# Performance work log

Measured on AMD Instinct MI355X. Metric: run time of the kernel, lower is better.

Reference implementation:

```python
import jax, jax.numpy as jnp
import numpy as np


def setup_inputs() -> dict:
    key = jax.random.key(0)
    k_fm, k_idx, k_x, k_y = jax.random.split(key, 4)
    N, C, H, W = 4, 256, 200, 272
    R = 1000
    feature_map = jax.random.normal(k_fm, (N, C, H, W), dtype=jnp.float32)
    img_idx = jax.random.randint(k_idx, (R,), 0, N, dtype=jnp.int32)
    # inclusive coords: x1<=x2<W, y1<=y2<H
    xs = jnp.sort(jax.random.randint(k_x, (R, 2), 0, W, dtype=jnp.int32), axis=1)
    ys = jnp.sort(jax.random.randint(k_y, (R, 2), 0, H, dtype=jnp.int32), axis=1)
    rois = jnp.stack([img_idx, xs[:, 0], ys[:, 0], xs[:, 1], ys[:, 1]], axis=1)
    return {"feature_map": feature_map, "rois": rois, "output_size": 7}


def reference(feature_map, rois, output_size):
    """ROI pooling with torch AdaptiveAvgPool2d semantics per crop.

    Bin i of a length-L crop averages rows [floor(i*L/O), ceil((i+1)*L/O)).
    Implemented exactly and fully vectorized via a 2D integral image, so no
    Python loop over ROIs and no dynamic shapes.
    """
    N, C, H, W = feature_map.shape
    O = output_size
    # integral image, zero-padded: integ[n,c,h,w] = sum of feature_map[n,c,:h,:w]
    integ = jnp.pad(
        jnp.cumsum(jnp.cumsum(feature_map, axis=2), axis=3),
        ((0, 0), (0, 0), (1, 0), (1, 0)),
    )
    img_idx = rois[:, 0]
    x1, y1, x2, y2 = rois[:, 1], rois[:, 2], rois[:, 3], rois[:, 4]
    h_in = y2 - y1 + 1  # inclusive coords -> crop size [R]
    w_in = x2 - x1 + 1
    b = jnp.arange(O, dtype=rois.dtype)
    # adaptive-pool bin edges (start inclusive, end exclusive), shape [R,O]
    hs = y1[:, None] + (b * h_in[:, None]) // O
    he = y1[:, None] + ((b + 1) * h_in[:, None] + O - 1) // O  # ceil div
    ws = x1[:, None] + (b * w_in[:, None]) // O
    we = x1[:, None] + ((b + 1) * w_in[:, None] + O - 1) // O
    n = img_idx[:, None, None]  # [R,1,1]

    def corner(hi, wi):
        # -> [R, O, O, C]
        return integ[n, :, hi[:, :, None], wi[:, None, :]]

    sums = corner(he, we) - corner(hs, we) - corner(he, ws) + corner(hs, ws)
    area = ((he - hs)[:, :, None] * (we - ws)[:, None, :]).astype(feature_map.dtype)
    out = (sums / area[..., None]).transpose(0, 3, 1, 2)  # [R, C, O, O]
    return img_idx, out
```

## Files before the change

### kernel.cpp

```cpp
#include <hip/hip_runtime.h>

#define NIMG 4
#define CCH  256
#define HDIM 200
#define WDIM 272
#define OSZ  7

__global__ __launch_bounds__(256) void k_rowscan(const float* __restrict__ fm,
                                                 float* __restrict__ integ) {
    const int c = threadIdx.x;
    const int b = blockIdx.x;
    const int n = b / HDIM;
    const int h = b % HDIM;

    const float4* src = reinterpret_cast<const float4*>(
        fm + ((size_t)((n * CCH + c) * HDIM + h)) * WDIM);
    float* dst = integ + ((size_t)(n * HDIM + h) * WDIM) * CCH + c;

    float acc = 0.0f;
#pragma unroll 4
    for (int w4 = 0; w4 < WDIM / 4; ++w4) {
        float4 v = src[w4];
        float a0 = acc + v.x;
        float a1 = a0 + v.y;
        float a2 = a1 + v.z;
        float a3 = a2 + v.w;
        size_t wb = (size_t)(w4 * 4) * CCH;
        dst[wb]            = a0;
        dst[wb + CCH]      = a1;
        dst[wb + 2 * CCH]  = a2;
        dst[wb + 3 * CCH]  = a3;
        acc = a3;
    }
}

__global__ __launch_bounds__(256) void k_colscan(float4* __restrict__ integ4) {
    const int C4 = CCH / 4;
    int t = blockIdx.x * 256 + threadIdx.x;
    int c4 = t & (C4 - 1);
    int rest = t >> 6;
    int w = rest % WDIM;
    int n = rest / WDIM;

    const int stride = WDIM * C4;
    int idx = ((n * HDIM) * WDIM + w) * C4 + c4;

    float4 run = make_float4(0.f, 0.f, 0.f, 0.f);
    for (int h = 0; h < HDIM; h += 2) {
        float4 v0 = integ4[idx];
        float4 v1 = integ4[idx + stride];
        run.x += v0.x; run.y += v0.y; run.z += v0.z; run.w += v0.w;
        integ4[idx] = run;
        run.x += v1.x; run.y += v1.y; run.z += v1.z; run.w += v1.w;
        integ4[idx + stride] = run;
        idx += 2 * stride;
    }
}

__global__ __launch_bounds__(256) void k_pool(const float* __restrict__ integ,
                                              const int* __restrict__ rois,
                                              float* __restrict__ out, int R) {
    const int b  = blockIdx.x;
    const int r  = b / (OSZ * OSZ);
    const int ij = b % (OSZ * OSZ);
    const int i  = ij / OSZ;
    const int j  = ij % OSZ;
    const int c  = threadIdx.x;

    const int* rp = rois + r * 5;
    const int n  = rp[0];
    const int x1 = rp[1], y1 = rp[2], x2 = rp[3], y2 = rp[4];
    const int h_in = y2 - y1 + 1;
    const int w_in = x2 - x1 + 1;

    const int hs = y1 + (i * h_in) / OSZ;
    const int he = y1 + ((i + 1) * h_in + OSZ - 1) / OSZ;
    const int ws = x1 + (j * w_in) / OSZ;
    const int we = x1 + ((j + 1) * w_in + OSZ - 1) / OSZ;

    const float inv_area = 1.0f / (float)((he - hs) * (we - ws));

    const int hi = he - 1, hl = hs - 1;
    const int wi = we - 1, wl = ws - 1;

    const float* base = integ + (size_t)n * HDIM * WDIM * CCH + c;

    float A = base[((size_t)hi * WDIM + wi) * CCH];
    float B = (hl >= 0) ? base[((size_t)hl * WDIM + wi) * CCH] : 0.0f;
    float Cv = (wl >= 0) ? base[((size_t)hi * WDIM + wl) * CCH] : 0.0f;
    float D = (hl >= 0 && wl >= 0) ? base[((size_t)hl * WDIM + wl) * CCH] : 0.0f;

    float s = (A - B) - (Cv - D);
    out[R + (((size_t)r * CCH + c) * OSZ + i) * OSZ + j] = s * inv_area;

    if (ij == 0 && c == 0) out[r] = (float)n;
}

__global__ __launch_bounds__(256) void k_direct(const float* __restrict__ fm,
                                                const int* __restrict__ rois,
                                                float* __restrict__ out, int R) {
    const int b  = blockIdx.x;
    const int r  = b / (OSZ * OSZ);
    const int ij = b % (OSZ * OSZ);
    const int i  = ij / OSZ;
    const int j  = ij % OSZ;
    const int c  = threadIdx.x;

    const int* rp = rois + r * 5;
    const int n  = rp[0];
    const int x1 = rp[1], y1 = rp[2], x2 = rp[3], y2 = rp[4];
    const int h_in = y2 - y1 + 1;
    const int w_in = x2 - x1 + 1;

    const int hs = y1 + (i * h_in) / OSZ;
    const int he = y1 + ((i + 1) * h_in + OSZ - 1) / OSZ;
    const int ws = x1 + (j * w_in) / OSZ;
    const int we = x1 + ((j + 1) * w_in + OSZ - 1) / OSZ;

    const float inv_area = 1.0f / (float)((he - hs) * (we - ws));

    const float* p = fm + (size_t)(n * CCH + c) * HDIM * WDIM;
    float acc = 0.0f;
    for (int h = hs; h < he; ++h) {
        const float* row = p + (size_t)h * WDIM;
        for (int w = ws; w < we; ++w) acc += row[w];
    }
    out[R + (((size_t)r * CCH + c) * OSZ + i) * OSZ + j] = acc * inv_area;

    if (ij == 0 && c == 0) out[r] = (float)n;
}

extern "C" void kernel_launch(void* const* d_in, const int* in_sizes, int n_in,
                              void* d_out, int out_size, void* d_ws, size_t ws_size,
                              hipStream_t stream) {
    const float* fm  = (const float*)d_in[0];
    const int* rois  = (const int*)d_in[1];
    float* out       = (float*)d_out;
    const int R      = in_sizes[1] / 5;

    const size_t need = (size_t)NIMG * HDIM * WDIM * CCH * sizeof(float);

    if (ws_size >= need) {
        float* integ = (float*)d_ws;
        k_rowscan<<<NIMG * HDIM, 256, 0, stream>>>(fm, integ);
        k_colscan<<<(NIMG * WDIM * (CCH / 4)) / 256, 256, 0, stream>>>((float4*)integ);
        k_pool<<<R * OSZ * OSZ, 256, 0, stream>>>(integ, rois, out, R);
    } else {
        k_direct<<<R * OSZ * OSZ, 256, 0, stream>>>(fm, rois, out, R);
    }
}
```

Before: 576.5 us.

## Split row scan into halves with carry fixup, batch column scan and pool per ROI

The row prefix scan is split into two half-width blocks per row. The left half's total is saved to a correction buffer, and the column scan adds that carry to the right-half columns, which doubles the parallelism of the row scan. The column scan now runs one block per (image, column) with 8-deep batched loads. Pooling is restructured so each block handles a whole ROI and writes all 49 bins contiguously per channel. The cost is an extra correction buffer, extra reads in the column scan, and larger register arrays in the pool kernel.

Result: faster. 502.9 us (-12.8%).

```diff
diff --git a/kernel.cpp b/kernel.cpp
--- a/kernel.cpp
+++ b/kernel.cpp
@@ -6,8 +6,41 @@
 #define WDIM 272
 #define OSZ  7
 
-__global__ __launch_bounds__(256) void k_rowscan(const float* __restrict__ fm,
-                                                 float* __restrict__ integ) {
+__global__ __launch_bounds__(256) void k_rowscan_half(const float* __restrict__ fm,
+                                                      float* __restrict__ integ,
+                                                      float* __restrict__ corr) {
+    const int c    = threadIdx.x;
+    const int b    = blockIdx.x;
+    const int half = b & 1;
+    const int nh   = b >> 1;
+    const int n    = nh / HDIM;
+    const int h    = nh % HDIM;
+    const int HW   = WDIM / 2;
+
+    const float4* src = reinterpret_cast<const float4*>(
+        fm + ((size_t)((n * CCH + c) * HDIM + h)) * WDIM + half * HW);
+    float* dst = integ + ((size_t)((n * HDIM + h) * WDIM) + half * HW) * CCH + c;
+
+    float acc = 0.0f;
+#pragma unroll 2
+    for (int w4 = 0; w4 < HW / 4; ++w4) {
+        float4 v = src[w4];
+        float a0 = acc + v.x;
+        float a1 = a0 + v.y;
+        float a2 = a1 + v.z;
+        float a3 = a2 + v.w;
+        size_t wb = (size_t)(w4 * 4) * CCH;
+        dst[wb]           = a0;
+        dst[wb + CCH]     = a1;
+        dst[wb + 2 * CCH] = a2;
+        dst[wb + 3 * CCH] = a3;
+        acc = a3;
+    }
+    if (half == 0) corr[(size_t)(n * HDIM + h) * CCH + c] = acc;
+}
+
+__global__ __launch_bounds__(256) void k_rowscan_full(const float* __restrict__ fm,
+                                                      float* __restrict__ integ) {
     const int c = threadIdx.x;
     const int b = blockIdx.x;
     const int n = b / HDIM;
@@ -18,7 +51,7 @@
     float* dst = integ + ((size_t)(n * HDIM + h) * WDIM) * CCH + c;
 
     float acc = 0.0f;
-#pragma unroll 4
+#pragma unroll 2
     for (int w4 = 0; w4 < WDIM / 4; ++w4) {
         float4 v = src[w4];
         float a0 = acc + v.x;
@@ -26,46 +59,47 @@
         float a2 = a1 + v.z;
         float a3 = a2 + v.w;
         size_t wb = (size_t)(w4 * 4) * CCH;
-        dst[wb]            = a0;
-        dst[wb + CCH]      = a1;
-        dst[wb + 2 * CCH]  = a2;
-        dst[wb + 3 * CCH]  = a3;
+        dst[wb]           = a0;
+        dst[wb + CCH]     = a1;
+        dst[wb + 2 * CCH] = a2;
+        dst[wb + 3 * CCH] = a3;
         acc = a3;
     }
 }
 
-__global__ __launch_bounds__(256) void k_colscan(float4* __restrict__ integ4) {
-    const int C4 = CCH / 4;
-    int t = blockIdx.x * 256 + threadIdx.x;
-    int c4 = t & (C4 - 1);
-    int rest = t >> 6;
-    int w = rest % WDIM;
-    int n = rest / WDIM;
-
-    const int stride = WDIM * C4;
-    int idx = ((n * HDIM) * WDIM + w) * C4 + c4;
-
-    float4 run = make_float4(0.f, 0.f, 0.f, 0.f);
-    for (int h = 0; h < HDIM; h += 2) {
-        float4 v0 = integ4[idx];
-        float4 v1 = integ4[idx + stride];
-        run.x += v0.x; run.y += v0.y; run.z += v0.z; run.w += v0.w;
-        integ4[idx] = run;
-        run.x += v1.x; run.y += v1.y; run.z += v1.z; run.w += v1.w;
-        integ4[idx + stride] = run;
-        idx += 2 * stride;
-    }
-}
-
-__global__ __launch_bounds__(256) void k_pool(const float* __restrict__ integ,
-                                              const int* __restrict__ rois,
-                                              float* __restrict__ out, int R) {
-    const int b  = blockIdx.x;
-    const int r  = b / (OSZ * OSZ);
-    const int ij = b % (OSZ * OSZ);
-    const int i  = ij / OSZ;
-    const int j  = ij % OSZ;
-    const int c  = threadIdx.x;
+template <bool HASCORR>
+__global__ __launch_bounds__(256) void k_colscan2(float* __restrict__ integ,
+                                                  const float* __restrict__ corr) {
+    const int b = blockIdx.x;
+    const int n = b / WDIM;
+    const int w = b % WDIM;
+    const int c = threadIdx.x;
+    const int S = WDIM * CCH;
+
+    float* p = integ + ((size_t)(n * HDIM) * WDIM + w) * CCH + c;
+    const float* cp = corr + (size_t)(n * HDIM) * CCH + c;
+    const bool right = HASCORR && (w >= WDIM / 2);
+
+    float run = 0.0f;
+    for (int h = 0; h < HDIM; h += 8) {
+        float v[8], u[8];
+#pragma unroll
+        for (int k = 0; k < 8; ++k) v[k] = p[(size_t)(h + k) * S];
+#pragma unroll
+        for (int k = 0; k < 8; ++k) u[k] = right ? cp[(size_t)(h + k) * CCH] : 0.0f;
+#pragma unroll
+        for (int k = 0; k < 8; ++k) {
+            run += v[k] + u[k];
+            p[(size_t)(h + k) * S] = run;
+        }
+    }
+}
+
+__global__ __launch_bounds__(256) void k_pool2(const float* __restrict__ integ,
+                                               const int* __restrict__ rois,
+                                               float* __restrict__ out, int R) {
+    const int r = blockIdx.x;
+    const int c = threadIdx.x;
 
     const int* rp = rois + r * 5;
     const int n  = rp[0];
@@ -73,27 +107,36 @@
     const int h_in = y2 - y1 + 1;
     const int w_in = x2 - x1 + 1;
 
-    const int hs = y1 + (i * h_in) / OSZ;
-    const int he = y1 + ((i + 1) * h_in + OSZ - 1) / OSZ;
-    const int ws = x1 + (j * w_in) / OSZ;
-    const int we = x1 + ((j + 1) * w_in + OSZ - 1) / OSZ;
-
-    const float inv_area = 1.0f / (float)((he - hs) * (we - ws));
-
-    const int hi = he - 1, hl = hs - 1;
-    const int wi = we - 1, wl = ws - 1;
-
     const float* base = integ + (size_t)n * HDIM * WDIM * CCH + c;
 
-    float A = base[((size_t)hi * WDIM + wi) * CCH];
-    float B = (hl >= 0) ? base[((size_t)hl * WDIM + wi) * CCH] : 0.0f;
-    float Cv = (wl >= 0) ? base[((size_t)hi * WDIM + wl) * CCH] : 0.0f;
-    float D = (hl >= 0 && wl >= 0) ? base[((size_t)hl * WDIM + wl) * CCH] : 0.0f;
-
-    float s = (A - B) - (Cv - D);
-    out[R + (((size_t)r * CCH + c) * OSZ + i) * OSZ + j] = s * inv_area;
-
-    if (ij == 0 && c == 0) out[r] = (float)n;
+    float res[OSZ * OSZ];
+#pragma unroll
+    for (int i = 0; i < OSZ; ++i) {
+        const int hs = y1 + (i * h_in) / OSZ;
+        const int he = y1 + ((i + 1) * h_in + OSZ - 1) / OSZ;
+        const int hl = hs - 1;
+        const size_t rhi = (size_t)(he - 1) * WDIM;
+        const size_t rhl = (size_t)hl * WDIM;
+#pragma unroll
+        for (int j = 0; j < OSZ; ++j) {
+            const int ws = x1 + (j * w_in) / OSZ;
+            const int we = x1 + ((j + 1) * w_in + OSZ - 1) / OSZ;
+            const int wl = ws - 1;
+            const int wi = we - 1;
+            float A  = base[(rhi + wi) * CCH];
+            float B  = (hl >= 0) ? base[(rhl + wi) * CCH] : 0.0f;
+            float Cv = (wl >= 0) ? base[(rhi + wl) * CCH] : 0.0f;
+            float D  = (hl >= 0 && wl >= 0) ? base[(rhl + wl) * CCH] : 0.0f;
+            const float inv_area = 1.0f / (float)((he - hs) * (we - ws));
+            res[i * OSZ + j] = ((A - B) - (Cv - D)) * inv_area;
+        }
+    }
+
+    float* po = out + R + (size_t)(r * CCH + c) * (OSZ * OSZ);
+#pragma unroll
+    for (int k = 0; k < OSZ * OSZ; ++k) po[k] = res[k];
+
+    if (c == 0) out[r] = (float)n;
 }
 
 __global__ __launch_bounds__(256) void k_direct(const float* __restrict__ fm,
@@ -138,13 +181,20 @@
     float* out       = (float*)d_out;
     const int R      = in_sizes[1] / 5;
 
-    const size_t need = (size_t)NIMG * HDIM * WDIM * CCH * sizeof(float);
-
-    if (ws_size >= need) {
+    const size_t need_integ = (size_t)NIMG * HDIM * WDIM * CCH * sizeof(float);
+    const size_t need_corr  = (size_t)NIMG * HDIM * CCH * sizeof(float);
+
+    if (ws_size >= need_integ + need_corr) {
         float* integ = (float*)d_ws;
-        k_rowscan<<<NIMG * HDIM, 256, 0, stream>>>(fm, integ);
-        k_colscan<<<(NIMG * WDIM * (CCH / 4)) / 256, 256, 0, stream>>>((float4*)integ);
-        k_pool<<<R * OSZ * OSZ, 256, 0, stream>>>(integ, rois, out, R);
+        float* corr  = integ + (size_t)NIMG * HDIM * WDIM * CCH;
+        k_rowscan_half<<<NIMG * HDIM * 2, 256, 0, stream>>>(fm, integ, corr);
+        k_colscan2<true><<<NIMG * WDIM, 256, 0, stream>>>(integ, corr);
+        k_pool2<<<R, 256, 0, stream>>>(integ, rois, out, R);
+    } else if (ws_size >= need_integ) {
+        float* integ = (float*)d_ws;
+        k_rowscan_full<<<NIMG * HDIM, 256, 0, stream>>>(fm, integ);
+        k_colscan2<false><<<NIMG * WDIM, 256, 0, stream>>>(integ, integ);
+        k_pool2<<<R, 256, 0, stream>>>(integ, rois, out, R);
     } else {
         k_direct<<<R * OSZ * OSZ, 256, 0, stream>>>(fm, rois, out, R);
     }
```

## Replace 2D integral image with column-only prefix and wave-scan pooling

Applied to the files above, without the earlier changes.

Drops the row scan and channel-last transpose. Builds only a column-wise cumulative sum in the native NCHW layout, then does the row prefix inside the pooling kernel with a wave-wide shuffle scan over each ROI's width. This removes one full read and write pass over the feature map and the strided transposed writes. In exchange, the pool kernel does far more work per ROI: one block per ROI, and every channel and bin row needs a scan over up to the full width.

Result: slower. 1.200 ms (+108.1%).

```diff
diff --git a/kernel.cpp b/kernel.cpp
--- a/kernel.cpp
+++ b/kernel.cpp
@@ -6,66 +6,31 @@
 #define WDIM 272
 #define OSZ  7
 
-__global__ __launch_bounds__(256) void k_rowscan(const float* __restrict__ fm,
-                                                 float* __restrict__ integ) {
-    const int c = threadIdx.x;
-    const int b = blockIdx.x;
-    const int n = b / HDIM;
-    const int h = b % HDIM;
+__global__ __launch_bounds__(256) void k_colscan_n(const float* __restrict__ fm,
+                                                   float* __restrict__ colint) {
+    const int gid = blockIdx.x * 256 + threadIdx.x;
+    const int w   = gid % WDIM;
+    const int nc  = gid / WDIM;
 
-    const float4* src = reinterpret_cast<const float4*>(
-        fm + ((size_t)((n * CCH + c) * HDIM + h)) * WDIM);
-    float* dst = integ + ((size_t)(n * HDIM + h) * WDIM) * CCH + c;
+    const float* src = fm     + (size_t)nc * HDIM * WDIM + w;
+    float*       dst = colint + (size_t)nc * HDIM * WDIM + w;
 
-    float acc = 0.0f;
-#pragma unroll 4
-    for (int w4 = 0; w4 < WDIM / 4; ++w4) {
-        float4 v = src[w4];
-        float a0 = acc + v.x;
-        float a1 = a0 + v.y;
-        float a2 = a1 + v.z;
-        float a3 = a2 + v.w;
-        size_t wb = (size_t)(w4 * 4) * CCH;
-        dst[wb]            = a0;
-        dst[wb + CCH]      = a1;
-        dst[wb + 2 * CCH]  = a2;
-        dst[wb + 3 * CCH]  = a3;
-        acc = a3;
+    float run = 0.0f;
+    for (int h = 0; h < HDIM; h += 8) {
+        float v[8];
+#pragma unroll
+        for (int k = 0; k < 8; ++k) v[k] = src[(size_t)(h + k) * WDIM];
+#pragma unroll
+        for (int k = 0; k < 8; ++k) { run += v[k]; dst[(size_t)(h + k) * WDIM] = run; }
     }
 }
 
-__global__ __launch_bounds__(256) void k_colscan(float4* __restrict__ integ4) {
-    const int C4 = CCH / 4;
-    int t = blockIdx.x * 256 + threadIdx.x;
-    int c4 = t & (C4 - 1);
-    int rest = t >> 6;
-    int w = rest % WDIM;
-    int n = rest / WDIM;
-
-    const int stride = WDIM * C4;
-    int idx = ((n * HDIM) * WDIM + w) * C4 + c4;
-
-    float4 run = make_float4(0.f, 0.f, 0.f, 0.f);
-    for (int h = 0; h < HDIM; h += 2) {
-        float4 v0 = integ4[idx];
-        float4 v1 = integ4[idx + stride];
-        run.x += v0.x; run.y += v0.y; run.z += v0.z; run.w += v0.w;
-        integ4[idx] = run;
-        run.x += v1.x; run.y += v1.y; run.z += v1.z; run.w += v1.w;
-        integ4[idx + stride] = run;
-        idx += 2 * stride;
-    }
-}
-
-__global__ __launch_bounds__(256) void k_pool(const float* __restrict__ integ,
-                                              const int* __restrict__ rois,
-                                              float* __restrict__ out, int R) {
-    const int b  = blockIdx.x;
-    const int r  = b / (OSZ * OSZ);
-    const int ij = b % (OSZ * OSZ);
-    const int i  = ij / OSZ;
-    const int j  = ij % OSZ;
-    const int c  = threadIdx.x;
+__global__ __launch_bounds__(256) void k_poolw(const float* __restrict__ colint,
+                                               const int* __restrict__ rois,
+                                               float* __restrict__ out, int R) {
+    const int r    = blockIdx.x;
+    const int lane = threadIdx.x & 63;
+    const int wave = threadIdx.x >> 6;
 
     const int* rp = rois + r * 5;
     const int n  = rp[0];
@@ -73,27 +38,95 @@
     const int h_in = y2 - y1 + 1;
     const int w_in = x2 - x1 + 1;
 
-    const int hs = y1 + (i * h_in) / OSZ;
-    const int he = y1 + ((i + 1) * h_in + OSZ - 1) / OSZ;
-    const int ws = x1 + (j * w_in) / OSZ;
-    const int we = x1 + ((j + 1) * w_in + OSZ - 1) / OSZ;
+    if (threadIdx.x == 0) out[r] = (float)n;
 
-    const float inv_area = 1.0f / (float)((he - hs) * (we - ws));
+    const int jl   = (lane < OSZ) ? lane : 0;
+    const int wsl  = x1 + (jl * w_in) / OSZ;
+    const int wel  = x1 + ((jl + 1) * w_in + OSZ - 1) / OSZ;
+    const int loTgt = wsl - 1;
+    const int hiTgt = wel - 1;
 
-    const int hi = he - 1, hl = hs - 1;
-    const int wi = we - 1, wl = ws - 1;
+    const int w0start = x1 & ~3;
+    const int nchunk  = (x2 - w0start) / 256 + 1;
 
-    const float* base = integ + (size_t)n * HDIM * WDIM * CCH + c;
+    const size_t img_base = (size_t)n * CCH * HDIM * WDIM;
 
-    float A = base[((size_t)hi * WDIM + wi) * CCH];
-    float B = (hl >= 0) ? base[((size_t)hl * WDIM + wi) * CCH] : 0.0f;
-    float Cv = (wl >= 0) ? base[((size_t)hi * WDIM + wl) * CCH] : 0.0f;
-    float D = (hl >= 0 && wl >= 0) ? base[((size_t)hl * WDIM + wl) * CCH] : 0.0f;
+    for (int t = wave; t < CCH * OSZ; t += 4) {
+        const int c = t / OSZ;
+        const int i = t - c * OSZ;
+        const int hs = y1 + (i * h_in) / OSZ;
+        const int he = y1 + ((i + 1) * h_in + OSZ - 1) / OSZ;
+        const float inv_area = 1.0f / (float)((he - hs) * (wel - wsl));
 
-    float s = (A - B) - (Cv - D);
-    out[R + (((size_t)r * CCH + c) * OSZ + i) * OSZ + j] = s * inv_area;
+        const float* rowT = colint + img_base + ((size_t)c * HDIM + (he - 1)) * WDIM;
+        const bool hasB = (hs > 0);
+        const float* rowB = hasB
+            ? colint + img_base + ((size_t)c * HDIM + (hs - 1)) * WDIM
+            : rowT;
 
-    if (ij == 0 && c == 0) out[r] = (float)n;
+        float lo = 0.0f, hi = 0.0f, runbase = 0.0f;
+
+        for (int ch = 0; ch < nchunk; ++ch) {
+            const int w0 = w0start + ch * 256;
+            const int lw = w0 + lane * 4;
+            const bool act = (lw <= x2);
+            const int addr = act ? lw : 0;
+
+            float4 tv = *reinterpret_cast<const float4*>(rowT + addr);
+            float4 bv = *reinterpret_cast<const float4*>(rowB + addr);
+            if (!hasB) bv = make_float4(0.f, 0.f, 0.f, 0.f);
+
+            float d0 = (act && lw     >= x1 && lw     <= x2) ? tv.x - bv.x : 0.0f;
+            float d1 = (act && lw + 1 >= x1 && lw + 1 <= x2) ? tv.y - bv.y : 0.0f;
+            float d2 = (act && lw + 2 >= x1 && lw + 2 <= x2) ? tv.z - bv.z : 0.0f;
+            float d3 = (act && lw + 3 >= x1 && lw + 3 <= x2) ? tv.w - bv.w : 0.0f;
+
+            const float s0 = d0, s1 = s0 + d1, s2 = s1 + d2, s3 = s2 + d3;
+
+            const float tot = s3;
+            float inc = tot;
+#pragma unroll
+            for (int off = 1; off < 64; off <<= 1) {
+                float y = __shfl_up(inc, off);
+                if (lane >= off) inc += y;
+            }
+            const float excl = inc - tot;
+
+            const float p0 = runbase + excl + s0;
+            const float p1 = runbase + excl + s1;
+            const float p2 = runbase + excl + s2;
+            const float p3 = runbase + excl + s3;
+
+            const float chunkTot = __shfl(inc, 63);
+
+            {
+                const int off_ = loTgt - w0;
+                const int sl   = (off_ >> 2) & 63;
+                const int k    = off_ & 3;
+                const float q0 = __shfl(p0, sl), q1 = __shfl(p1, sl);
+                const float q2 = __shfl(p2, sl), q3 = __shfl(p3, sl);
+                const float v01 = (k & 1) ? q1 : q0;
+                const float v23 = (k & 1) ? q3 : q2;
+                if (off_ >= 0 && off_ < 256) lo = (k & 2) ? v23 : v01;
+            }
+            {
+                const int off_ = hiTgt - w0;
+                const int sl   = (off_ >> 2) & 63;
+                const int k    = off_ & 3;
+                const float q0 = __shfl(p0, sl), q1 = __shfl(p1, sl);
+                const float q2 = __shfl(p2, sl), q3 = __shfl(p3, sl);
+                const float v01 = (k & 1) ? q1 : q0;
+                const float v23 = (k & 1) ? q3 : q2;
+                if (off_ >= 0 && off_ < 256) hi = (k & 2) ? v23 : v01;
+            }
+            runbase += chunkTot;
+        }
+
+        if (lane < OSZ) {
+            out[(size_t)R + (((size_t)r * CCH + c) * OSZ + i) * OSZ + lane] =
+                (hi - lo) * inv_area;
+        }
+    }
 }
 
 __global__ __launch_bounds__(256) void k_direct(const float* __restrict__ fm,
@@ -138,13 +171,12 @@
     float* out       = (float*)d_out;
     const int R      = in_sizes[1] / 5;
 
-    const size_t need = (size_t)NIMG * HDIM * WDIM * CCH * sizeof(float);
+    const size_t need = (size_t)NIMG * CCH * HDIM * WDIM * sizeof(float);
 
     if (ws_size >= need) {
-        float* integ = (float*)d_ws;
-        k_rowscan<<<NIMG * HDIM, 256, 0, stream>>>(fm, integ);
-        k_colscan<<<(NIMG * WDIM * (CCH / 4)) / 256, 256, 0, stream>>>((float4*)integ);
-        k_pool<<<R * OSZ * OSZ, 256, 0, stream>>>(integ, rois, out, R);
+        float* colint = (float*)d_ws;
+        k_colscan_n<<<(NIMG * CCH * WDIM) / 256, 256, 0, stream>>>(fm, colint);
+        k_poolw<<<R, 256, 0, stream>>>(colint, rois, out, R);
     } else {
         k_direct<<<R * OSZ * OSZ, 256, 0, stream>>>(fm, rois, out, R);
     }
```
